# Kernel tuning notes

Hardware: AMD Instinct MI355X
Metric: run time of the kernel (lower is better)

## Reference

```python
import jax, jax.numpy as jnp
from jax import lax
import numpy as np

T, B, D, H, L, HO, OUT = 256, 4096, 32, 256, 32, 512, 8
DELTA = 1.0  # delta_next


def setup_inputs() -> dict:
    key = jax.random.key(0)
    ks = jax.random.split(key, 20)
    g = lambda i, shape, s: jax.random.normal(ks[i], shape, jnp.float32) * s
    x_history = jax.random.normal(ks[0], (T, B, D), jnp.float32)
    # strictly increasing times, identical across batch (as in a shared grid)
    t_history = jnp.broadcast_to((jnp.arange(T, dtype=jnp.float32) * 0.1)[:, None, None], (T, B, 1))
    inp = {
        "x_history": x_history,
        "t_history": t_history,
        # GRU (PyTorch gate order r,z,n), stored as (in, 3H)
        "W_ih": g(1, (D + 1, 3 * H), 0.05), "W_hh": g(2, (H, 3 * H), 0.05),
        "b_ih": jnp.zeros((3 * H,), jnp.float32), "b_hh": jnp.zeros((3 * H,), jnp.float32),
        # hid2lat
        "W_lat": g(3, (H, 2 * L), 0.05), "b_lat": jnp.zeros((2 * L,), jnp.float32),
        # ODE func 3-layer tanh MLP (xavier gain 0.1 in original -> small init)
        "W1": g(4, (L, HO), 0.02), "b1": jnp.zeros((HO,), jnp.float32),
        "W2": g(5, (HO, HO), 0.02), "b2": jnp.zeros((HO,), jnp.float32),
        "W3": g(6, (HO, L), 0.02), "b3": jnp.zeros((L,), jnp.float32),
        # decoder
        "Wd1": g(7, (L, H), 0.05), "bd1": jnp.zeros((H,), jnp.float32),
        "Wd2": g(8, (H, OUT), 0.05), "bd2": jnp.zeros((OUT,), jnp.float32),
    }
    return inp


def reference(x_history, t_history, W_ih, W_hh, b_ih, b_hh, W_lat, b_lat,
              W1, b1, W2, b2, W3, b3, Wd1, bd1, Wd2, bd2):
    latent = b_lat.shape[0] // 2
    # dt: dt[0]=0, dt[i]=t[i]-t[i-1]
    dt = jnp.concatenate([jnp.zeros_like(t_history[:1]), t_history[1:] - t_history[:-1]], axis=0)
    xt = jnp.concatenate([x_history, dt], axis=-1)          # [T, B, D+1]
    seq = xt[::-1]                                           # GRU over flipped sequence

    def gru_step(h, x_t):
        gi = x_t @ W_ih + b_ih                               # [B, 3H]
        gh = h @ W_hh + b_hh
        i_r, i_z, i_n = jnp.split(gi, 3, axis=-1)
        h_r, h_z, h_n = jnp.split(gh, 3, axis=-1)
        r = jax.nn.sigmoid(i_r + h_r)
        z = jax.nn.sigmoid(i_z + h_z)
        n = jnp.tanh(i_n + r * h_n)
        return (1.0 - z) * n + z * h, None

    h0 = jnp.zeros((x_history.shape[1], W_hh.shape[0]), x_history.dtype)
    hT, _ = lax.scan(gru_step, h0, seq)
    z0 = (hT @ W_lat + b_lat)[:, :latent]                    # z_mean, [B, L]

    def f(z):  # ODE func: 3-layer tanh MLP, t-independent
        return jnp.tanh(jnp.tanh(z @ W1 + b1) @ W2 + b2) @ W3 + b3

    # torchdiffeq 'rk4' = single 3/8-rule step over [t0, t0+DELTA]
    hstep = jnp.asarray(DELTA, z0.dtype)
    k1 = f(z0)
    k2 = f(z0 + hstep * k1 / 3.0)
    k3 = f(z0 + hstep * (k2 - k1 / 3.0))
    k4 = f(z0 + hstep * (k1 - k2 + k3))
    zT = z0 + hstep * (k1 + 3.0 * k2 + 3.0 * k3 + k4) / 8.0

    return jax.nn.relu(zT @ Wd1 + bd1) @ Wd2 + bd2           # [B, OUT]
```

## Files before the change

kernel.cpp:

```cpp
#include <hip/hip_runtime.h>

typedef _Float16 f16;
typedef _Float16 h8 __attribute__((ext_vector_type(8)));
typedef float f32x4 __attribute__((ext_vector_type(4)));

#define MFMA16(a,b,c) __builtin_amdgcn_mfma_f32_16x16x32_f16((a),(b),(c),0,0,0)
#define MFMA8(a,b,c)  __builtin_amdgcn_mfma_f32_16x16x32_fp8_bf8((long)(a),(long)(b),(c),0,0,0)

#define TT 256
#define BB 4096
#define OUTD 8

#define WS_WHH    0u
#define WS_WIHHI  393216u
#define WS_WIHLO  442368u
#define WS_WLON   466944u
#define WS_WLAT   532480u
#define WS_W1T    548864u
#define WS_W2T    581632u
#define WS_W3T    1105920u
#define WS_WD1T   1138688u
#define WS_WD2T   1155072u

#define L_HB     0
#define L_WRT    16384
#define L_CST    147456
#define LDS_SIZE 155648

__device__ __forceinline__ float fsigm(float x) {
  return __builtin_amdgcn_rcpf(1.f + __builtin_amdgcn_exp2f(-1.44269504f * x));
}
__device__ __forceinline__ float ftanh(float x) {
  return 1.f - 2.f * __builtin_amdgcn_rcpf(1.f + __builtin_amdgcn_exp2f(2.88539008f * x));
}
__device__ __forceinline__ f32x4 splat4(float v) { f32x4 r = {v, v, v, v}; return r; }

__device__ __forceinline__ long long pack_e4m3_h8(h8 a) {
  int lo = __builtin_amdgcn_cvt_pk_fp8_f32((float)a[0], (float)a[1], 0, false);
  lo = __builtin_amdgcn_cvt_pk_fp8_f32((float)a[2], (float)a[3], lo, true);
  int hi = __builtin_amdgcn_cvt_pk_fp8_f32((float)a[4], (float)a[5], 0, false);
  hi = __builtin_amdgcn_cvt_pk_fp8_f32((float)a[6], (float)a[7], hi, true);
  return (long long)(unsigned)lo | ((long long)hi << 32);
}
__device__ __forceinline__ long long pack_e4m3_f32x8(f32x4 a, f32x4 b) {
  int lo = __builtin_amdgcn_cvt_pk_fp8_f32(a[0], a[1], 0, false);
  lo = __builtin_amdgcn_cvt_pk_fp8_f32(a[2], a[3], lo, true);
  int hi = __builtin_amdgcn_cvt_pk_fp8_f32(b[0], b[1], 0, false);
  hi = __builtin_amdgcn_cvt_pk_fp8_f32(b[2], b[3], hi, true);
  return (long long)(unsigned)lo | ((long long)hi << 32);
}

__global__ __launch_bounds__(512) void prep_kernel(
    const float* __restrict__ Wih, const float* __restrict__ Whh,
    const float* __restrict__ Wlat, const float* __restrict__ W1,
    const float* __restrict__ W2, const float* __restrict__ W3,
    const float* __restrict__ Wd1, const float* __restrict__ Wd2,
    char* __restrict__ ws) {
  int idx = blockIdx.x * 512 + threadIdx.x;
  if (idx < 768*256) {
    int n = idx >> 8, k = idx & 255;
    ((f16*)(ws + WS_WHH))[n*256 + k] = (f16)(Whh[k*768 + n] * 256.f);
  }
  if (idx < 768*32) {
    int n = idx >> 5, k = idx & 31;
    ((f16*)(ws + WS_WIHHI))[n*32 + k] = (f16)(Wih[k*768 + n] * 256.f);
  }
  if (idx < 768*16) {
    int n = idx >> 4, k2 = (idx & 15) * 2;
    float w0 = Wih[k2*768 + n] * 256.f;
    float w1 = Wih[(k2+1)*768 + n] * 256.f;
    float r0 = w0 - (float)(f16)w0;
    float r1 = w1 - (float)(f16)w1;
    int p = __builtin_amdgcn_cvt_pk_bf8_f32(r0, r1, 0, false);
    *(short*)(ws + WS_WIHLO + n*32 + k2) = (short)p;
  }
  if (idx < 256*128) {
    int n = idx >> 7, k2 = (idx & 127) * 2;
    int c = 512 + n;
    float w0 = Whh[k2*768 + c] * 256.f;
    float w1 = Whh[(k2+1)*768 + c] * 256.f;
    float r0 = w0 - (float)(f16)w0;
    float r1 = w1 - (float)(f16)w1;
    int p = __builtin_amdgcn_cvt_pk_bf8_f32(r0, r1, 0, false);
    *(short*)(ws + WS_WLON + n*256 + k2) = (short)p;
  }
  if (idx < 32*256)  { int n = idx >> 8, k = idx & 255; ((f16*)(ws + WS_WLAT))[n*256 + k] = (f16)Wlat[k*64 + n]; }
  if (idx < 512*32)  { int n = idx >> 5, k = idx & 31;  ((f16*)(ws + WS_W1T))[n*32 + k]   = (f16)W1[k*512 + n]; }
  if (idx < 512*512) { int n = idx >> 9, k = idx & 511; ((f16*)(ws + WS_W2T))[n*512 + k]  = (f16)W2[k*512 + n]; }
  if (idx < 32*512)  { int n = idx >> 9, k = idx & 511; ((f16*)(ws + WS_W3T))[n*512 + k]  = (f16)W3[k*32 + n]; }
  if (idx < 256*32)  { int n = idx >> 5, k = idx & 31;  ((f16*)(ws + WS_WD1T))[n*32 + k]  = (f16)Wd1[k*256 + n]; }
  if (idx < 16*256)  { int n = idx >> 8, k = idx & 255; ((f16*)(ws + WS_WD2T))[n*256 + k] = (n < 8) ? (f16)Wd2[k*8 + n] : (f16)0.f; }
}

__global__ __launch_bounds__(512) void gru_ode_kernel(
    const float* __restrict__ xh, const float* __restrict__ th,
    const float* __restrict__ Wih_f, const float* __restrict__ bih,
    const float* __restrict__ bhh, const float* __restrict__ blat,
    const float* __restrict__ b1, const float* __restrict__ b2,
    const float* __restrict__ b3, const float* __restrict__ bd1,
    const float* __restrict__ bd2, const char* __restrict__ ws,
    float* __restrict__ out) {
  extern __shared__ char smem[];
  char* HB  = smem + L_HB;
  char* WRT = smem + L_WRT;
  float* CST = (float*)(smem + L_CST);
  const char* wlng = ws + WS_WLON;
  const char* wilg = ws + WS_WIHLO;
  const char* wihg = ws + WS_WIHHI;

  const int tid  = threadIdx.x;
  const int wave = tid >> 6;
  const int lane = tid & 63;
  const int lq   = lane >> 4;
  const int lr   = lane & 15;
  const int m0   = blockIdx.x << 4;
  const int swz  = (lr & 7) << 4;
  const int lq16 = lq * 16, lq8 = lq * 8;
  const float S  = 1.f / 256.f;

  #pragma unroll
  for (int it = 0; it < 8; ++it) ((unsigned*)HB)[tid + it*512] = 0u;
  {
    #pragma unroll
    for (int it = 0; it < 64; ++it) {
      int i = tid + it*512;
      int row = i >> 7, kw = i & 127;
      unsigned v = *(const unsigned*)(ws + WS_WHH + row*512 + kw*4);
      *(unsigned*)(WRT + row*512 + ((kw*4) ^ ((row & 7) << 4))) = v;
    }
  }
  if (tid < 256) {
    int c = tid;
    CST[c*7 + 0] = Wih_f[32*768 + c];
    CST[c*7 + 1] = Wih_f[32*768 + 256 + c];
    CST[c*7 + 2] = Wih_f[32*768 + 512 + c];
    CST[c*7 + 3] = bih[c] + bhh[c];
    CST[c*7 + 4] = bih[256 + c] + bhh[256 + c];
    CST[c*7 + 5] = bih[512 + c];
    CST[c*7 + 6] = bhh[512 + c];
  }

  h8 Wfz[2][8], Wfn[2][8];
  #pragma unroll
  for (int t = 0; t < 2; ++t) {
    const char* bz = ws + WS_WHH + (256 + wave*32 + t*16 + lr)*512 + lq16;
    const char* bn = ws + WS_WHH + (512 + wave*32 + t*16 + lr)*512 + lq16;
    #pragma unroll
    for (int kc = 0; kc < 8; ++kc) {
      Wfz[t][kc] = *(const h8*)(bz + kc*64);
      Wfn[t][kc] = *(const h8*)(bn + kc*64);
    }
  }

  float hreg[2][4];
  #pragma unroll
  for (int t = 0; t < 2; ++t)
    #pragma unroll
    for (int r = 0; r < 4; ++r) hreg[t][r] = 0.f;

  const int wrt0 = (wave*32 + lr)*512;
  const int wln0 = (wave*32 + lr)*256;

  __syncthreads();

  #pragma unroll 1
  for (int s = 0; s < 256; ++s) {
    const int tsrc = 255 - s;
    f32x4 xa = *(const f32x4*)(xh + (size_t)(tsrc*BB + m0 + lr)*32 + lq8);
    f32x4 xb = *(const f32x4*)(xh + (size_t)(tsrc*BB + m0 + lr)*32 + lq8 + 4);
    f32x4 tha = *(const f32x4*)(th + tsrc*BB + m0 + lq*4);
    f32x4 thb = tha;
    if (tsrc > 0) thb = *(const f32x4*)(th + (tsrc-1)*BB + m0 + lq*4);

    f32x4 accR[2], accZ[2], accNH[2], accNI[2];
    #pragma unroll
    for (int t = 0; t < 2; ++t) { accR[t] = splat4(0.f); accZ[t] = splat4(0.f); accNH[t] = splat4(0.f); accNI[t] = splat4(0.f); }

    #pragma unroll
    for (int kc = 0; kc < 8; ++kc) {
      const int ko = (kc*64 + lq16) ^ swz;
      h8 ahi = *(const h8*)(HB + lr*1024 + ko);
      h8 alo = *(const h8*)(HB + lr*1024 + 512 + ko);
      h8 wr0 = *(const h8*)(WRT + wrt0 + ko);
      h8 wr1 = *(const h8*)(WRT + wrt0 + 8192 + ko);
      accR[0] = MFMA16(ahi, wr0, accR[0]);       accR[0] = MFMA16(alo, wr0, accR[0]);
      accR[1] = MFMA16(ahi, wr1, accR[1]);       accR[1] = MFMA16(alo, wr1, accR[1]);
      accZ[0] = MFMA16(ahi, Wfz[0][kc], accZ[0]); accZ[0] = MFMA16(alo, Wfz[0][kc], accZ[0]);
      accZ[1] = MFMA16(ahi, Wfz[1][kc], accZ[1]); accZ[1] = MFMA16(alo, Wfz[1][kc], accZ[1]);
      accNH[0] = MFMA16(ahi, Wfn[0][kc], accNH[0]); accNH[0] = MFMA16(alo, Wfn[0][kc], accNH[0]);
      accNH[1] = MFMA16(ahi, Wfn[1][kc], accNH[1]); accNH[1] = MFMA16(alo, Wfn[1][kc], accNH[1]);
      long long a8 = pack_e4m3_h8(ahi);
      long long b80 = *(const long long*)(wlng + wln0 + kc*32 + lq8);
      long long b81 = *(const long long*)(wlng + wln0 + 4096 + kc*32 + lq8);
      accNH[0] = MFMA8(a8, b80, accNH[0]);
      accNH[1] = MFMA8(a8, b81, accNH[1]);
    }

    h8 xhi, xlo;
    #pragma unroll
    for (int j = 0; j < 8; ++j) {
      float v = (j < 4) ? xa[j] : xb[j-4];
      f16 h = (f16)v;
      xhi[j] = h; xlo[j] = (f16)(v - (float)h);
    }
    long long ax8 = pack_e4m3_f32x8(xa, xb);
    #pragma unroll
    for (int t = 0; t < 2; ++t) {
      int nr =       wave*32 + t*16 + lr;
      int nz = 256 + wave*32 + t*16 + lr;
      int nn = 512 + wave*32 + t*16 + lr;
      h8 br_ = *(const h8*)(wihg + nr*64 + lq16);
      h8 bz_ = *(const h8*)(wihg + nz*64 + lq16);
      h8 bn_ = *(const h8*)(wihg + nn*64 + lq16);
      accR[t]  = MFMA16(xhi, br_, accR[t]);  accR[t]  = MFMA16(xlo, br_, accR[t]);
      accZ[t]  = MFMA16(xhi, bz_, accZ[t]);  accZ[t]  = MFMA16(xlo, bz_, accZ[t]);
      accNI[t] = MFMA16(xhi, bn_, accNI[t]); accNI[t] = MFMA16(xlo, bn_, accNI[t]);
      long long br8 = *(const long long*)(wilg + nr*32 + lq8);
      long long bz8 = *(const long long*)(wilg + nz*32 + lq8);
      long long bn8 = *(const long long*)(wilg + nn*32 + lq8);
      accR[t]  = MFMA8(ax8, br8, accR[t]);
      accZ[t]  = MFMA8(ax8, bz8, accZ[t]);
      accNI[t] = MFMA8(ax8, bn8, accNI[t]);
    }

    __syncthreads();

    float dtv[4];
    #pragma unroll
    for (int r = 0; r < 4; ++r) dtv[r] = tha[r] - thb[r];
    #pragma unroll
    for (int t = 0; t < 2; ++t) {
      int c = wave*32 + t*16 + lr;
      const float* cc = CST + c*7;
      float w32r = cc[0], w32z = cc[1], w32n = cc[2];
      float br = cc[3], bz = cc[4], bin = cc[5], bhn = cc[6];
      #pragma unroll
      for (int r = 0; r < 4; ++r) {
        float rv = accR[t][r]*S + br + dtv[r]*w32r;
        float zv = accZ[t][r]*S + bz + dtv[r]*w32z;
        float iv = accNI[t][r]*S + bin + dtv[r]*w32n;
        float hn = accNH[t][r]*S + bhn;
        float rg = fsigm(rv), zg = fsigm(zv);
        float nv = ftanh(iv + rg*hn);
        float hv = nv + zg*(hreg[t][r] - nv);
        hreg[t][r] = hv;
        int row = lq*4 + r;
        f16 hh = (f16)hv;
        *(f16*)(HB + row*1024 + ((2*c) ^ ((row & 7) << 4))) = hh;
        *(f16*)(HB + row*1024 + 512 + ((2*c) ^ ((row & 7) << 4))) = (f16)(hv - (float)hh);
      }
    }
    __syncthreads();
  }

  f32x4 z0a = splat4(blat[lr]);
  f32x4 z0b = splat4(blat[16 + lr]);
  #pragma unroll
  for (int kc = 0; kc < 8; ++kc) {
    h8 ahi = *(const h8*)(HB + lr*1024 + ((kc*64 + lq16) ^ swz));
    h8 alo = *(const h8*)(HB + lr*1024 + 512 + ((kc*64 + lq16) ^ swz));
    h8 ba = *(const h8*)(ws + WS_WLAT + lr*512 + kc*64 + lq16);
    h8 bb = *(const h8*)(ws + WS_WLAT + (16 + lr)*512 + kc*64 + lq16);
    z0a = MFMA16(ahi, ba, z0a); z0a = MFMA16(alo, ba, z0a);
    z0b = MFMA16(ahi, bb, z0b); z0b = MFMA16(alo, bb, z0b);
  }

  char* TZ  = smem + L_WRT;
  char* TU1 = smem + L_WRT + 2048;
  char* TU2 = smem + L_WRT + 18432;
  char* TD  = smem + L_WRT + 34816;

  auto Ffun = [&](f32x4 zina, f32x4 zinb, f32x4& ka, f32x4& kb) {
    if (wave == 0) {
      #pragma unroll
      for (int r = 0; r < 4; ++r) {
        int row = lq*4 + r;
        *(f16*)(TZ + row*64 + ((2*lr) ^ ((row & 3) << 4))) = (f16)zina[r];
        *(f16*)(TZ + row*64 + ((2*(16 + lr)) ^ ((row & 3) << 4))) = (f16)zinb[r];
      }
    }
    __syncthreads();
    h8 za = *(const h8*)(TZ + lr*64 + ((lq16) ^ ((lr & 3) << 4)));
    #pragma unroll
    for (int st = 0; st < 4; ++st) {
      int n = wave*64 + st*16 + lr;
      f32x4 t0 = splat4(b1[n]);
      t0 = MFMA16(za, *(const h8*)(ws + WS_W1T + n*64 + lq16), t0);
      #pragma unroll
      for (int r = 0; r < 4; ++r) {
        int row = lq*4 + r;
        *(f16*)(TU1 + row*1024 + ((2*n) ^ ((row & 7) << 4))) = (f16)ftanh(t0[r]);
      }
    }
    __syncthreads();
    #pragma unroll
    for (int st = 0; st < 4; ++st) {
      int n = wave*64 + st*16 + lr;
      f32x4 t0 = splat4(b2[n]);
      #pragma unroll
      for (int kc = 0; kc < 16; ++kc) {
        h8 a = *(const h8*)(TU1 + lr*1024 + ((kc*64 + lq16) ^ ((lr & 7) << 4)));
        t0 = MFMA16(a, *(const h8*)(ws + WS_W2T + n*1024 + kc*64 + lq16), t0);
      }
      #pragma unroll
      for (int r = 0; r < 4; ++r) {
        int row = lq*4 + r;
        *(f16*)(TU2 + row*1024 + ((2*n) ^ ((row & 7) << 4))) = (f16)ftanh(t0[r]);
      }
    }
    __syncthreads();
    f32x4 t0 = splat4(b3[lr]), t1 = splat4(b3[16 + lr]);
    #pragma unroll
    for (int kc = 0; kc < 16; ++kc) {
      h8 a = *(const h8*)(TU2 + lr*1024 + ((kc*64 + lq16) ^ ((lr & 7) << 4)));
      t0 = MFMA16(a, *(const h8*)(ws + WS_W3T + lr*1024 + kc*64 + lq16), t0);
      t1 = MFMA16(a, *(const h8*)(ws + WS_W3T + (16 + lr)*1024 + kc*64 + lq16), t1);
    }
    ka = t0; kb = t1;
    __syncthreads();
  };

  f32x4 k1a, k1b, k2a, k2b, k3a, k3b, k4a, k4b;
  Ffun(z0a, z0b, k1a, k1b);
  Ffun(z0a + k1a*(1.f/3.f), z0b + k1b*(1.f/3.f), k2a, k2b);
  Ffun(z0a + k2a - k1a*(1.f/3.f), z0b + k2b - k1b*(1.f/3.f), k3a, k3b);
  Ffun(z0a + k1a - k2a + k3a, z0b + k1b - k2b + k3b, k4a, k4b);
  f32x4 zTa = z0a + (k1a + 3.f*k2a + 3.f*k3a + k4a)*0.125f;
  f32x4 zTb = z0b + (k1b + 3.f*k2b + 3.f*k3b + k4b)*0.125f;

  if (wave == 0) {
    #pragma unroll
    for (int r = 0; r < 4; ++r) {
      int row = lq*4 + r;
      *(f16*)(TZ + row*64 + ((2*lr) ^ ((row & 3) << 4))) = (f16)zTa[r];
      *(f16*)(TZ + row*64 + ((2*(16 + lr)) ^ ((row & 3) << 4))) = (f16)zTb[r];
    }
  }
  __syncthreads();
  {
    h8 za = *(const h8*)(TZ + lr*64 + ((lq16) ^ ((lr & 3) << 4)));
    #pragma unroll
    for (int st = 0; st < 2; ++st) {
      int n = wave*32 + st*16 + lr;
      f32x4 t0 = splat4(bd1[n]);
      t0 = MFMA16(za, *(const h8*)(ws + WS_WD1T + n*64 + lq16), t0);
      #pragma unroll
      for (int r = 0; r < 4; ++r) {
        int row = lq*4 + r;
        float v = t0[r] > 0.f ? t0[r] : 0.f;
        *(f16*)(TD + row*512 + ((2*n) ^ ((row & 7) << 4))) = (f16)v;
      }
    }
  }
  __syncthreads();
  if (wave == 0) {
    f32x4 o = splat4(0.f);
    #pragma unroll
    for (int kc = 0; kc < 8; ++kc) {
      h8 a = *(const h8*)(TD + lr*512 + ((kc*64 + lq16) ^ ((lr & 7) << 4)));
      o = MFMA16(a, *(const h8*)(ws + WS_WD2T + lr*512 + kc*64 + lq16), o);
    }
    if (lr < OUTD) {
      float q = bd2[lr];
      #pragma unroll
      for (int r = 0; r < 4; ++r) out[(m0 + lq*4 + r)*OUTD + lr] = o[r] + q;
    }
  }
}

extern "C" void kernel_launch(void* const* d_in, const int* in_sizes, int n_in,
                              void* d_out, int out_size, void* d_ws, size_t ws_size,
                              hipStream_t stream) {
  const float* x    = (const float*)d_in[0];
  const float* th   = (const float*)d_in[1];
  const float* Wih  = (const float*)d_in[2];
  const float* Whh  = (const float*)d_in[3];
  const float* bih  = (const float*)d_in[4];
  const float* bhh  = (const float*)d_in[5];
  const float* Wlat = (const float*)d_in[6];
  const float* blat = (const float*)d_in[7];
  const float* W1   = (const float*)d_in[8];
  const float* b1   = (const float*)d_in[9];
  const float* W2   = (const float*)d_in[10];
  const float* b2   = (const float*)d_in[11];
  const float* W3   = (const float*)d_in[12];
  const float* b3   = (const float*)d_in[13];
  const float* Wd1  = (const float*)d_in[14];
  const float* bd1  = (const float*)d_in[15];
  const float* Wd2  = (const float*)d_in[16];
  const float* bd2  = (const float*)d_in[17];
  (void)in_sizes; (void)n_in; (void)out_size; (void)ws_size;

  static int lds_set = 0;
  if (!lds_set) {
    hipFuncSetAttribute((const void*)gru_ode_kernel,
                        hipFuncAttributeMaxDynamicSharedMemorySize, LDS_SIZE);
    lds_set = 1;
  }

  prep_kernel<<<512, 512, 0, stream>>>(Wih, Whh, Wlat, W1, W2, W3, Wd1, Wd2, (char*)d_ws);
  gru_ode_kernel<<<256, 512, LDS_SIZE, stream>>>(x, th, Wih, bih, bhh, blat, b1, b2, b3,
                                                 bd1, bd2, (const char*)d_ws, (float*)d_out);
}
```

Measured before the change: 2.561 ms.

## Double-buffer GRU hidden state in LDS to drop one barrier per step

The hidden-state LDS buffer becomes two ping-pong buffers, so each recurrent step reads the current buffer and writes the next one. That removes the barrier that separated the MFMA reads from the state writes, leaving one barrier per step, implemented as an explicit lgkmcnt wait plus s_barrier. The per-column gate constants (dt weights and biases) move from an LDS table into per-thread registers, removing LDS loads in the gate epilogue. The cost is more register pressure in an already register-heavy kernel and a larger LDS footprint.

Result: slower. 2.622 ms (+2.4%).

```diff
diff --git a/kernel.cpp b/kernel.cpp
--- a/kernel.cpp
+++ b/kernel.cpp
@@ -6,6 +6,9 @@
 
 #define MFMA16(a,b,c) __builtin_amdgcn_mfma_f32_16x16x32_f16((a),(b),(c),0,0,0)
 #define MFMA8(a,b,c)  __builtin_amdgcn_mfma_f32_16x16x32_fp8_bf8((long)(a),(long)(b),(c),0,0,0)
+
+#define BARLDS() do { asm volatile("s_waitcnt lgkmcnt(0)" ::: "memory"); \
+                      __builtin_amdgcn_s_barrier(); } while (0)
 
 #define TT 256
 #define BB 4096
@@ -22,10 +25,9 @@
 #define WS_WD1T   1138688u
 #define WS_WD2T   1155072u
 
-#define L_HB     0
-#define L_WRT    16384
-#define L_CST    147456
-#define LDS_SIZE 155648
+#define L_WRT    0
+#define L_HB     131072
+#define LDS_SIZE 163840
 
 __device__ __forceinline__ float fsigm(float x) {
   return __builtin_amdgcn_rcpf(1.f + __builtin_amdgcn_exp2f(-1.44269504f * x));
@@ -101,9 +103,8 @@
     const float* __restrict__ bd2, const char* __restrict__ ws,
     float* __restrict__ out) {
   extern __shared__ char smem[];
+  char* WRT = smem + L_WRT;
   char* HB  = smem + L_HB;
-  char* WRT = smem + L_WRT;
-  float* CST = (float*)(smem + L_CST);
   const char* wlng = ws + WS_WLON;
   const char* wilg = ws + WS_WIHLO;
   const char* wihg = ws + WS_WIHHI;
@@ -119,7 +120,7 @@
   const float S  = 1.f / 256.f;
 
   #pragma unroll
-  for (int it = 0; it < 8; ++it) ((unsigned*)HB)[tid + it*512] = 0u;
+  for (int it = 0; it < 16; ++it) ((unsigned*)HB)[tid + it*512] = 0u;
   {
     #pragma unroll
     for (int it = 0; it < 64; ++it) {
@@ -129,15 +130,18 @@
       *(unsigned*)(WRT + row*512 + ((kw*4) ^ ((row & 7) << 4))) = v;
     }
   }
-  if (tid < 256) {
-    int c = tid;
-    CST[c*7 + 0] = Wih_f[32*768 + c];
-    CST[c*7 + 1] = Wih_f[32*768 + 256 + c];
-    CST[c*7 + 2] = Wih_f[32*768 + 512 + c];
-    CST[c*7 + 3] = bih[c] + bhh[c];
-    CST[c*7 + 4] = bih[256 + c] + bhh[256 + c];
-    CST[c*7 + 5] = bih[512 + c];
-    CST[c*7 + 6] = bhh[512 + c];
+
+  float cw[2][7];
+  #pragma unroll
+  for (int t = 0; t < 2; ++t) {
+    int c = wave*32 + t*16 + lr;
+    cw[t][0] = Wih_f[32*768 + c];
+    cw[t][1] = Wih_f[32*768 + 256 + c];
+    cw[t][2] = Wih_f[32*768 + 512 + c];
+    cw[t][3] = bih[c] + bhh[c];
+    cw[t][4] = bih[256 + c] + bhh[256 + c];
+    cw[t][5] = bih[512 + c];
+    cw[t][6] = bhh[512 + c];
   }
 
   h8 Wfz[2][8], Wfn[2][8];
@@ -166,6 +170,9 @@
   #pragma unroll 1
   for (int s = 0; s < 256; ++s) {
     const int tsrc = 255 - s;
+    char* cur = HB + ((s & 1) << 14);
+    char* nxt = HB + (((s + 1) & 1) << 14);
+
     f32x4 xa = *(const f32x4*)(xh + (size_t)(tsrc*BB + m0 + lr)*32 + lq8);
     f32x4 xb = *(const f32x4*)(xh + (size_t)(tsrc*BB + m0 + lr)*32 + lq8 + 4);
     f32x4 tha = *(const f32x4*)(th + tsrc*BB + m0 + lq*4);
@@ -179,8 +186,8 @@
     #pragma unroll
     for (int kc = 0; kc < 8; ++kc) {
       const int ko = (kc*64 + lq16) ^ swz;
-      h8 ahi = *(const h8*)(HB + lr*1024 + ko);
-      h8 alo = *(const h8*)(HB + lr*1024 + 512 + ko);
+      h8 ahi = *(const h8*)(cur + lr*1024 + ko);
+      h8 alo = *(const h8*)(cur + lr*1024 + 512 + ko);
       h8 wr0 = *(const h8*)(WRT + wrt0 + ko);
       h8 wr1 = *(const h8*)(WRT + wrt0 + 8192 + ko);
       accR[0] = MFMA16(ahi, wr0, accR[0]);       accR[0] = MFMA16(alo, wr0, accR[0]);
@@ -223,17 +230,14 @@
       accNI[t] = MFMA8(ax8, bn8, accNI[t]);
     }
 
-    __syncthreads();
-
     float dtv[4];
     #pragma unroll
     for (int r = 0; r < 4; ++r) dtv[r] = tha[r] - thb[r];
     #pragma unroll
     for (int t = 0; t < 2; ++t) {
       int c = wave*32 + t*16 + lr;
-      const float* cc = CST + c*7;
-      float w32r = cc[0], w32z = cc[1], w32n = cc[2];
-      float br = cc[3], bz = cc[4], bin = cc[5], bhn = cc[6];
+      float w32r = cw[t][0], w32z = cw[t][1], w32n = cw[t][2];
+      float br = cw[t][3], bz = cw[t][4], bin = cw[t][5], bhn = cw[t][6];
       #pragma unroll
       for (int r = 0; r < 4; ++r) {
         float rv = accR[t][r]*S + br + dtv[r]*w32r;
@@ -246,11 +250,11 @@
         hreg[t][r] = hv;
         int row = lq*4 + r;
         f16 hh = (f16)hv;
-        *(f16*)(HB + row*1024 + ((2*c) ^ ((row & 7) << 4))) = hh;
-        *(f16*)(HB + row*1024 + 512 + ((2*c) ^ ((row & 7) << 4))) = (f16)(hv - (float)hh);
-      }
-    }
-    __syncthreads();
+        *(f16*)(nxt + row*1024 + ((2*c) ^ ((row & 7) << 4))) = hh;
+        *(f16*)(nxt + row*1024 + 512 + ((2*c) ^ ((row & 7) << 4))) = (f16)(hv - (float)hh);
+      }
+    }
+    BARLDS();
   }
 
   f32x4 z0a = splat4(blat[lr]);
@@ -265,10 +269,10 @@
     z0b = MFMA16(ahi, bb, z0b); z0b = MFMA16(alo, bb, z0b);
   }
 
-  char* TZ  = smem + L_WRT;
-  char* TU1 = smem + L_WRT + 2048;
-  char* TU2 = smem + L_WRT + 18432;
-  char* TD  = smem + L_WRT + 34816;
+  char* TZ  = smem + 0;
+  char* TU1 = smem + 2048;
+  char* TU2 = smem + 18432;
+  char* TD  = smem + 34816;
 
   auto Ffun = [&](f32x4 zina, f32x4 zinb, f32x4& ka, f32x4& kb) {
     if (wave == 0) {
```
